# Kernel optimization log

Hardware: AMD Instinct MI355X
Metric: run time of the kernel (lower is better)

Reference implementation:

```python
import jax, jax.numpy as jnp
import numpy as np

# --- sampler hyperparameters (from init_kwargs) ---
NUM_SAMPLES = 8
NUM_EXP = 256
OVER_SAMPLE_RATE = 1.5
NUM_SAMPLES_BOUNDARY = 40
DTIME_MAX = 5.0
NUM_EVENT_TYPES = 20
NUM_MARK = 10
B, S = 32, 512


def _intensity(event_seq, sample_times, emb, scale, bias):
    """Synthetic multivariate intensity: [B,S,N] times -> [B,S,N,NUM_MARK]."""
    e = emb[event_seq]  # [B,S,M] gather by event type (irregular access)
    return jax.nn.softplus(e[:, :, None, :] + scale * jnp.cos(sample_times)[..., None] + bias)


def setup_inputs() -> dict:
    key = jax.random.key(0)
    ks = jax.random.split(key, 6)
    dt = jax.random.uniform(ks[0], (B, S), dtype=jnp.float32) + 1e-3  # positive deltas
    t = jnp.cumsum(dt, axis=1)  # monotone timestamps
    ev = jax.random.randint(ks[1], (B, S), 0, NUM_EVENT_TYPES, dtype=jnp.int64)
    # raw Exp(1) draws (inverse-CDF of uniform)
    u = jax.random.uniform(ks[2], (B, S, NUM_EXP), dtype=jnp.float32, minval=1e-7, maxval=1.0)
    exp_raw = -jnp.log(u)
    unif = jax.random.uniform(ks[3], (B, S, NUM_SAMPLES, NUM_EXP), dtype=jnp.float32)
    emb = jax.random.normal(ks[4], (NUM_EVENT_TYPES, NUM_MARK), dtype=jnp.float32)
    scale = jax.random.normal(ks[5], (NUM_MARK,), dtype=jnp.float32) * 0.5
    bias = jnp.zeros((NUM_MARK,), dtype=jnp.float32)
    return {"time_seq": t, "time_delta_seq": dt, "event_seq": ev,
            "exp_raw": exp_raw, "unif_numbers": unif,
            "emb": emb, "scale": scale, "bias": bias}


def reference(time_seq, time_delta_seq, event_seq, exp_raw, unif_numbers, emb, scale, bias):
    # --- compute_intensity_upper_bound (compute_last_step_only=False) ---
    lin = jnp.linspace(0.0, 1.0, NUM_SAMPLES_BOUNDARY, dtype=jnp.float32)  # [K]
    t_bound = time_seq[:, :, None] + time_delta_seq[:, :, None] * lin[None, None, :]  # [B,S,K]
    lam_bound = _intensity(event_seq, t_bound, emb, scale, bias)  # [B,S,K,M]
    upper = jnp.max(lam_bound.sum(-1), axis=-1) * OVER_SAMPLE_RATE  # [B,S]

    # --- sample_exp_distribution ---
    exp_numbers = exp_raw / upper[:, :, None]  # [B,S,E]

    # --- intensities at sampled times ---
    time_exp = time_seq[:, :, None] + exp_numbers  # [B,S,E]
    total_int = _intensity(event_seq, time_exp, emb, scale, bias).sum(-1)  # [B,S,E]

    # --- sample_accept (broadcast instead of tile) ---
    criterion = unif_numbers * upper[:, :, None, None] / total_int[:, :, None, :]  # [B,S,NS,E]
    accept = criterion < 1.0
    masked_exp = jnp.where(accept, exp_numbers[:, :, None, :], jnp.inf)
    min_time = jnp.min(masked_exp, axis=3)  # [B,S,NS] first-accepted = smallest accepted dt
    res = jnp.where(jnp.isinf(min_time), jnp.float32(DTIME_MAX), min_time)
    res = jnp.minimum(res, 1e5)
    weights = jnp.ones_like(res) / res.shape[2]
    return res, weights
```

## Files before the change

kernel.cpp:

```cpp
#include <hip/hip_runtime.h>
#include <math.h>

#define NBATCH 32
#define NSEQ 512
#define NSAMP 8
#define NEXP 256
#define KBOUND 40
#define NMARK 10
#define DTIME_MAX 5.0f
#define OVER_SAMPLE 1.5f

__device__ __forceinline__ float fast_cos(float x) {
    constexpr double inv2pi_d = 0.15915494309189535;
    constexpr float chi = (float)inv2pi_d;
    constexpr float clo = (float)(inv2pi_d - (double)chi);
    float n = rintf(x * chi);
    float f = fmaf(x, chi, -n);
    f = fmaf(x, clo, f);
    return __builtin_amdgcn_cosf(f);
}

__device__ __forceinline__ float intensity_sum(float c, const float eb[NMARK],
                                               const float sc[NMARK]) {
    const float NLOG2E = -1.4426950408889634f;
    const float LN2    =  0.69314718055994531f;
    float acc0 = 0.f, acc1 = 0.f, p0 = 1.f, p1 = 1.f;
    #pragma unroll
    for (int m = 0; m < NMARK; m += 2) {
        float x0 = fmaf(sc[m],     c, eb[m]);
        float x1 = fmaf(sc[m + 1], c, eb[m + 1]);
        float e0 = __builtin_amdgcn_exp2f(fabsf(x0) * NLOG2E);
        float e1 = __builtin_amdgcn_exp2f(fabsf(x1) * NLOG2E);
        p0 *= (1.f + e0);
        p1 *= (1.f + e1);
        acc0 += fmaxf(x0, 0.f);
        acc1 += fmaxf(x1, 0.f);
    }
    return fmaf(LN2, __builtin_amdgcn_logf(p0 * p1), acc0 + acc1);
}

__device__ __forceinline__ float rfl_f(float x) {
    return __int_as_float(__builtin_amdgcn_readfirstlane(__float_as_int(x)));
}

__global__ __launch_bounds__(256) void syn_event_sampler(
    const float* __restrict__ time_seq,
    const float* __restrict__ dt_seq,
    const int*   __restrict__ event_seq,
    const float* __restrict__ exp_raw,
    const float* __restrict__ unif,
    const float* __restrict__ emb,
    const float* __restrict__ scale,
    const float* __restrict__ bias,
    float* __restrict__ out_res,
    float* __restrict__ out_w)
{
    const int lane = threadIdx.x & 63;
    const int wv   = threadIdx.x >> 6;
    const int bs   = blockIdx.x * 4 + wv;

    const float4 er4 = *reinterpret_cast<const float4*>(
        exp_raw + (size_t)bs * NEXP + 4 * lane);
    const float* ub = unif + (size_t)bs * NSAMP * NEXP + 4 * lane;
    float4 u4[NSAMP];
    #pragma unroll
    for (int ns = 0; ns < NSAMP; ++ns)
        u4[ns] = *reinterpret_cast<const float4*>(ub + (size_t)ns * NEXP);

    const float t   = rfl_f(time_seq[bs]);
    const float dtv = rfl_f(dt_seq[bs]);
    const int   ev  = __builtin_amdgcn_readfirstlane(event_seq[bs]);

    float eb[NMARK], sc[NMARK];
    #pragma unroll
    for (int m = 0; m < NMARK; ++m) {
        eb[m] = emb[ev * NMARK + m] + bias[m];
        sc[m] = scale[m];
    }

    float bsum = -INFINITY;
    if (lane < KBOUND) {
        const float step = 1.0f / 39.0f;
        float tb = __fadd_rn(t, __fmul_rn(dtv, __fmul_rn((float)lane, step)));
        bsum = intensity_sum(fast_cos(tb), eb, sc);
    }
    #pragma unroll
    for (int off = 1; off < 64; off <<= 1)
        bsum = fmaxf(bsum, __shfl_xor(bsum, off, 64));
    const float upper = bsum * OVER_SAMPLE;

    float expn[4], total[4];
    expn[0] = er4.x / upper;  expn[1] = er4.y / upper;
    expn[2] = er4.z / upper;  expn[3] = er4.w / upper;
    #pragma unroll
    for (int i = 0; i < 4; ++i)
        total[i] = intensity_sum(fast_cos(t + expn[i]), eb, sc);

    float vmin[NSAMP];
    #pragma unroll
    for (int ns = 0; ns < NSAMP; ++ns) {
        float c0 = (__fmul_rn(u4[ns].x, upper) < total[0]) ? expn[0] : INFINITY;
        float c1 = (__fmul_rn(u4[ns].y, upper) < total[1]) ? expn[1] : INFINITY;
        float c2 = (__fmul_rn(u4[ns].z, upper) < total[2]) ? expn[2] : INFINITY;
        float c3 = (__fmul_rn(u4[ns].w, upper) < total[3]) ? expn[3] : INFINITY;
        float v = fminf(fminf(c0, c1), fminf(c2, c3));
        #pragma unroll
        for (int off = 1; off < 64; off <<= 1)
            v = fminf(v, __shfl_xor(v, off, 64));
        vmin[ns] = v;
    }

    float rv = vmin[0];
    #pragma unroll
    for (int ns = 1; ns < NSAMP; ++ns)
        rv = (lane == ns) ? vmin[ns] : rv;
    if (lane < NSAMP) {
        float r = isinf(rv) ? DTIME_MAX : rv;
        r = fminf(r, 1e5f);
        out_res[(size_t)bs * NSAMP + lane] = r;
        out_w  [(size_t)bs * NSAMP + lane] = 1.0f / NSAMP;
    }
}

extern "C" void kernel_launch(void* const* d_in, const int* in_sizes, int n_in,
                              void* d_out, int out_size, void* d_ws, size_t ws_size,
                              hipStream_t stream) {
    const float* time_seq = (const float*)d_in[0];
    const float* dt_seq   = (const float*)d_in[1];
    const int*   ev_seq   = (const int*)  d_in[2];
    const float* exp_raw  = (const float*)d_in[3];
    const float* unif     = (const float*)d_in[4];
    const float* emb      = (const float*)d_in[5];
    const float* scale    = (const float*)d_in[6];
    const float* bias     = (const float*)d_in[7];

    float* out_res = (float*)d_out;
    float* out_w   = out_res + (size_t)NBATCH * NSEQ * NSAMP;

    dim3 grid((NBATCH * NSEQ) / 4);
    dim3 block(256);
    syn_event_sampler<<<grid, block, 0, stream>>>(
        time_seq, dt_seq, ev_seq, exp_raw, unif, emb, scale, bias, out_res, out_w);
}
```

Baseline: 213.9 us.

## Split fused sampler into three kernels staged through workspace

```diff
diff --git a/kernel.cpp b/kernel.cpp
--- a/kernel.cpp
+++ b/kernel.cpp
@@ -9,6 +9,11 @@
 #define NMARK 10
 #define DTIME_MAX 5.0f
 #define OVER_SAMPLE 1.5f
+#define NBS (NBATCH * NSEQ)
+
+#define WS_UPPER 0
+#define WS_EXPN  (1 << 20)
+#define WS_TOTAL (12 << 20)
 
 __device__ __forceinline__ float fast_cos(float x) {
     constexpr double inv2pi_d = 0.15915494309189535;
@@ -43,40 +48,31 @@
     return __int_as_float(__builtin_amdgcn_readfirstlane(__float_as_int(x)));
 }
 
-__global__ __launch_bounds__(256) void syn_event_sampler(
-    const float* __restrict__ time_seq,
-    const float* __restrict__ dt_seq,
-    const int*   __restrict__ event_seq,
-    const float* __restrict__ exp_raw,
-    const float* __restrict__ unif,
-    const float* __restrict__ emb,
-    const float* __restrict__ scale,
-    const float* __restrict__ bias,
-    float* __restrict__ out_res,
-    float* __restrict__ out_w)
-{
-    const int lane = threadIdx.x & 63;
-    const int wv   = threadIdx.x >> 6;
-    const int bs   = blockIdx.x * 4 + wv;
-
-    const float4 er4 = *reinterpret_cast<const float4*>(
-        exp_raw + (size_t)bs * NEXP + 4 * lane);
-    const float* ub = unif + (size_t)bs * NSAMP * NEXP + 4 * lane;
-    float4 u4[NSAMP];
-    #pragma unroll
-    for (int ns = 0; ns < NSAMP; ++ns)
-        u4[ns] = *reinterpret_cast<const float4*>(ub + (size_t)ns * NEXP);
-
-    const float t   = rfl_f(time_seq[bs]);
-    const float dtv = rfl_f(dt_seq[bs]);
-    const int   ev  = __builtin_amdgcn_readfirstlane(event_seq[bs]);
-
-    float eb[NMARK], sc[NMARK];
+__device__ __forceinline__ void load_marks(const float* __restrict__ emb,
+                                           const float* __restrict__ scale,
+                                           const float* __restrict__ bias,
+                                           int ev, float eb[NMARK], float sc[NMARK]) {
     #pragma unroll
     for (int m = 0; m < NMARK; ++m) {
         eb[m] = emb[ev * NMARK + m] + bias[m];
         sc[m] = scale[m];
     }
+}
+
+__global__ __launch_bounds__(256) void k_upper(
+    const float* __restrict__ time_seq, const float* __restrict__ dt_seq,
+    const int* __restrict__ event_seq,
+    const float* __restrict__ emb, const float* __restrict__ scale,
+    const float* __restrict__ bias, float* __restrict__ ws)
+{
+    const int lane = threadIdx.x & 63;
+    const int bs   = blockIdx.x * 4 + (threadIdx.x >> 6);
+
+    const float t   = rfl_f(time_seq[bs]);
+    const float dtv = rfl_f(dt_seq[bs]);
+    const int   ev  = __builtin_amdgcn_readfirstlane(event_seq[bs]);
+    float eb[NMARK], sc[NMARK];
+    load_marks(emb, scale, bias, ev, eb, sc);
 
     float bsum = -INFINITY;
     if (lane < KBOUND) {
@@ -87,23 +83,69 @@
     #pragma unroll
     for (int off = 1; off < 64; off <<= 1)
         bsum = fmaxf(bsum, __shfl_xor(bsum, off, 64));
-    const float upper = bsum * OVER_SAMPLE;
+    if (lane == 0) ws[WS_UPPER + bs] = bsum * OVER_SAMPLE;
+}
 
-    float expn[4], total[4];
-    expn[0] = er4.x / upper;  expn[1] = er4.y / upper;
-    expn[2] = er4.z / upper;  expn[3] = er4.w / upper;
+__global__ __launch_bounds__(256) void k_sample(
+    const float* __restrict__ time_seq, const int* __restrict__ event_seq,
+    const float* __restrict__ exp_raw,
+    const float* __restrict__ emb, const float* __restrict__ scale,
+    const float* __restrict__ bias, float* __restrict__ ws)
+{
+    const int lane = threadIdx.x & 63;
+    const int bs   = blockIdx.x * 4 + (threadIdx.x >> 6);
+
+    const float4 er4 = *reinterpret_cast<const float4*>(
+        exp_raw + (size_t)bs * NEXP + 4 * lane);
+
+    const float t     = rfl_f(time_seq[bs]);
+    const float upper = rfl_f(ws[WS_UPPER + bs]);
+    const int   ev    = __builtin_amdgcn_readfirstlane(event_seq[bs]);
+    float eb[NMARK], sc[NMARK];
+    load_marks(emb, scale, bias, ev, eb, sc);
+
+    float4 ex, to;
+    ex.x = er4.x / upper;  ex.y = er4.y / upper;
+    ex.z = er4.z / upper;  ex.w = er4.w / upper;
+    to.x = intensity_sum(fast_cos(t + ex.x), eb, sc);
+    to.y = intensity_sum(fast_cos(t + ex.y), eb, sc);
+    to.z = intensity_sum(fast_cos(t + ex.z), eb, sc);
+    to.w = intensity_sum(fast_cos(t + ex.w), eb, sc);
+
+    *reinterpret_cast<float4*>(ws + WS_EXPN  + (size_t)bs * NEXP + 4 * lane) = ex;
+    *reinterpret_cast<float4*>(ws + WS_TOTAL + (size_t)bs * NEXP + 4 * lane) = to;
+}
+
+__global__ __launch_bounds__(256) void k_accept(
+    const float* __restrict__ unif, const float* __restrict__ ws,
+    float* __restrict__ out_res, float* __restrict__ out_w)
+{
+    const int lane = threadIdx.x & 63;
+    const int bs   = blockIdx.x * 4 + (threadIdx.x >> 6);
+
+    const float* ub = unif + (size_t)bs * NSAMP * NEXP + 4 * lane;
+    float4 u4[NSAMP];
     #pragma unroll
-    for (int i = 0; i < 4; ++i)
-        total[i] = intensity_sum(fast_cos(t + expn[i]), eb, sc);
+    for (int ns = 0; ns < NSAMP; ++ns)
+        u4[ns] = *reinterpret_cast<const float4*>(ub + (size_t)ns * NEXP);
+    const float4 ex = *reinterpret_cast<const float4*>(
+        ws + WS_EXPN + (size_t)bs * NEXP + 4 * lane);
+    const float4 to = *reinterpret_cast<const float4*>(
+        ws + WS_TOTAL + (size_t)bs * NEXP + 4 * lane);
+    const float upper = rfl_f(ws[WS_UPPER + bs]);
 
     float vmin[NSAMP];
     #pragma unroll
     for (int ns = 0; ns < NSAMP; ++ns) {
-        float c0 = (__fmul_rn(u4[ns].x, upper) < total[0]) ? expn[0] : INFINITY;
-        float c1 = (__fmul_rn(u4[ns].y, upper) < total[1]) ? expn[1] : INFINITY;
-        float c2 = (__fmul_rn(u4[ns].z, upper) < total[2]) ? expn[2] : INFINITY;
-        float c3 = (__fmul_rn(u4[ns].w, upper) < total[3]) ? expn[3] : INFINITY;
-        float v = fminf(fminf(c0, c1), fminf(c2, c3));
+        float c0 = (__fmul_rn(u4[ns].x, upper) < to.x) ? ex.x : INFINITY;
+        float c1 = (__fmul_rn(u4[ns].y, upper) < to.y) ? ex.y : INFINITY;
+        float c2 = (__fmul_rn(u4[ns].z, upper) < to.z) ? ex.z : INFINITY;
+        float c3 = (__fmul_rn(u4[ns].w, upper) < to.w) ? ex.w : INFINITY;
+        vmin[ns] = fminf(fminf(c0, c1), fminf(c2, c3));
+    }
+    #pragma unroll
+    for (int ns = 0; ns < NSAMP; ++ns) {
+        float v = vmin[ns];
         #pragma unroll
         for (int off = 1; off < 64; off <<= 1)
             v = fminf(v, __shfl_xor(v, off, 64));
@@ -134,11 +176,12 @@
     const float* scale    = (const float*)d_in[6];
     const float* bias     = (const float*)d_in[7];
 
+    float* ws      = (float*)d_ws;
     float* out_res = (float*)d_out;
-    float* out_w   = out_res + (size_t)NBATCH * NSEQ * NSAMP;
+    float* out_w   = out_res + (size_t)NBS * NSAMP;
 
-    dim3 grid((NBATCH * NSEQ) / 4);
-    dim3 block(256);
-    syn_event_sampler<<<grid, block, 0, stream>>>(
-        time_seq, dt_seq, ev_seq, exp_raw, unif, emb, scale, bias, out_res, out_w);
+    dim3 grid(NBS / 4), block(256);
+    k_upper <<<grid, block, 0, stream>>>(time_seq, dt_seq, ev_seq, emb, scale, bias, ws);
+    k_sample<<<grid, block, 0, stream>>>(time_seq, ev_seq, exp_raw, emb, scale, bias, ws);
+    k_accept<<<grid, block, 0, stream>>>(unif, ws, out_res, out_w);
 }
```

Result: slower. 228.6 us (+6.9%).
